# Optimization experiments

Measured on AMD Instinct MI355X. Metric: run time of the kernel, lower is better.

Reference implementation:

```python
import jax, jax.numpy as jnp
import numpy as np

K = 32            # neighbors per node
LAMBDA_REG = 0.1  # geodesic regularization weight
TEMP = 0.1        # softmax temperature


def setup_inputs() -> dict:
    key = jax.random.key(0)
    features = jax.random.normal(key, (8192, 128), dtype=jnp.float32)
    return {"features": features}


def reference(features):
    # features: [B, D]
    B, D = features.shape
    k = K

    # cosine-normalized similarity (F.normalize with eps=1e-12)
    fnorm = jnp.linalg.norm(features, axis=1, keepdims=True)        # [B, 1]
    x = features / jnp.maximum(fnorm, 1e-12)
    sim = x @ x.T                                                    # [B, B]

    # dynamic kNN graph: top-(k+1), drop self (first column)
    _, topk_idx = jax.lax.top_k(sim, k + 1)                          # [B, k+1]
    dst = topk_idx[:, 1:].reshape(-1)                                # [B*k]
    src = jnp.repeat(jnp.arange(B), k)                               # [B*k]
    rows = jnp.concatenate([src, dst])                               # [2*B*k]
    cols = jnp.concatenate([dst, src])

    # symmetric degree normalization (deg computed from src only, as in torch)
    deg = jax.ops.segment_sum(jnp.ones(B * k, jnp.float32), src, num_segments=B)
    dis = jnp.where(deg > 0, 1.0 / jnp.sqrt(jnp.maximum(deg, 1.0)), 0.0)
    w = dis[rows] * dis[cols]                                        # [2*B*k]

    def spmm(v):
        # sparse COO matmul: duplicate (row,col) entries sum, matching torch sparse
        return jax.ops.segment_sum(v[cols] * w[:, None], rows, num_segments=B)

    diff1 = spmm(features)          # A @ features
    geodesic = spmm(diff1)          # A @ (A @ features)

    # pairwise cosine similarity features vs geodesic (torch eps=1e-8)
    gnorm = jnp.linalg.norm(geodesic, axis=1)                        # [B]
    denom = jnp.maximum(fnorm * gnorm[None, :], 1e-8)                # [B, B]
    cos = (features @ geodesic.T) / denom

    raw_weights = sim + LAMBDA_REG * cos
    weights = jax.nn.softmax(raw_weights / TEMP, axis=-1)            # [B, B]
    enhanced = weights @ features                                    # [B, D]
    return enhanced
```

## Files before the change

kernel.cpp:

```cpp
#include <hip/hip_runtime.h>
#include <hip/hip_bf16.h>

typedef unsigned short u16;
typedef unsigned int u32;
typedef __attribute__((ext_vector_type(8))) short bf16x8;
typedef __attribute__((ext_vector_type(4))) float f32x4;

#define LOG2E 1.4426950408889634f
#define B_N 8192
#define D_DIM 128
#define KNN 32
#define CAP_P 28
#define NPART 16
#define TAU 0.19f

__device__ __forceinline__ u16 f2b(float f) {
    unsigned u = __float_as_uint(f);
    unsigned r = (u + 0x7fffu + ((u >> 16) & 1u)) >> 16;
    return (u16)r;
}
__device__ __forceinline__ float b2f(u16 h) { return __uint_as_float((u32)h << 16); }

__device__ __forceinline__ f32x4 mfma16(bf16x8 a, bf16x8 b, f32x4 c) {
    return __builtin_amdgcn_mfma_f32_16x16x32_bf16(a, b, c, 0, 0, 0);
}

__device__ __forceinline__ size_t pk_off(int i, int d) {
    int T = i >> 5, r = ((i >> 4) & 1) * 4 + (d >> 5);
    int lane = ((d >> 3) & 3) * 16 + (i & 15);
    return ((size_t)((T * 8 + r) * 64 + lane)) * 8 + (d & 7);
}

__global__ __launch_bounds__(128) void prep_kernel(const float* __restrict__ f,
                                                   u16* __restrict__ xb, u16* __restrict__ xbp) {
    int i = blockIdx.x, d = threadIdx.x;
    float v = f[i * D_DIM + d];
    float ss = v * v;
#pragma unroll
    for (int m = 1; m < 64; m <<= 1) ss += __shfl_xor(ss, m, 64);
    __shared__ float wsum[2];
    if ((d & 63) == 0) wsum[d >> 6] = ss;
    __syncthreads();
    float nrm = sqrtf(wsum[0] + wsum[1]);
    u16 b = f2b(v / fmaxf(nrm, 1e-12f));
    xb[i * D_DIM + d] = b;
    xbp[pk_off(i, d)] = b;
}

__global__ __launch_bounds__(256) void vtp_kernel(const float* __restrict__ f, u16* __restrict__ vtp) {
    __shared__ u16 tile[32][130];
    int T = blockIdx.x, t = threadIdx.x;
    for (int idx = t; idx < 32 * 128; idx += 256) {
        int ir = idx >> 7, d = idx & 127;
        tile[ir][d] = f2b(f[(size_t)(T * 32 + ir) * D_DIM + d]);
    }
    __syncthreads();
#pragma unroll
    for (int cc = 0; cc < 2; cc++) {
        int c = t + cc * 256;
        int db = c >> 6, lane = c & 63;
        u16 out[8];
#pragma unroll
        for (int j = 0; j < 8; j++)
            out[j] = tile[(lane >> 4) * 8 + j][db * 16 + (lane & 15)];
        *(bf16x8*)(vtp + (size_t)(T * 512 + c) * 8) = *(bf16x8*)out;
    }
}

__global__ __launch_bounds__(512, 1) void cand_kernel(const u16* __restrict__ xb, const u16* __restrict__ xbp,
                                                      u32* __restrict__ candk, int* __restrict__ candcnt) {
    __shared__ int cnt_s[256];
    int tid = threadIdx.x;
    int wave = tid >> 6, lane = tid & 63, l15 = lane & 15, l4 = lane >> 4;
    int part = blockIdx.y;
    int qrow0 = blockIdx.x * 256 + wave * 32;
    if (tid < 256) cnt_s[tid] = 0;
    __syncthreads();

    bf16x8 a[2][4];
#pragma unroll
    for (int rt = 0; rt < 2; rt++) {
        const u16* arow = xb + (size_t)(qrow0 + rt * 16 + l15) * D_DIM + l4 * 8;
#pragma unroll
        for (int kk = 0; kk < 4; kk++) a[rt][kk] = *(const bf16x8*)(arow + kk * 32);
    }

    auto ldb = [&](bf16x8 (&bfr)[2][4], int j0) {
        const u16* bp = xbp + ((size_t)(j0 >> 5) * 8) * 512 + lane * 8;
#pragma unroll
        for (int ct = 0; ct < 2; ct++)
#pragma unroll
            for (int kk = 0; kk < 4; kk++) bfr[ct][kk] = *(const bf16x8*)(bp + (ct * 4 + kk) * 512);
    };
    auto proc = [&](bf16x8 (&bfr)[2][4], int j0) {
#pragma unroll
        for (int rt = 0; rt < 2; rt++) {
            f32x4 s0 = {0.f, 0.f, 0.f, 0.f}, s1 = {0.f, 0.f, 0.f, 0.f};
#pragma unroll
            for (int kk = 0; kk < 4; kk++) {
                s0 = mfma16(a[rt][kk], bfr[0][kk], s0);
                s1 = mfma16(a[rt][kk], bfr[1][kk], s1);
            }
#pragma unroll
            for (int r = 0; r < 4; r++) {
                int rloc = wave * 32 + rt * 16 + 4 * l4 + r;
                int gi = blockIdx.x * 256 + rloc;
#pragma unroll
                for (int ct = 0; ct < 2; ct++) {
                    float v = ct ? s1[r] : s0[r];
                    int gj = j0 + ct * 16 + l15;
                    if (v >= TAU && gj != gi) {
                        int slot = atomicAdd(&cnt_s[rloc], 1);
                        if (slot < CAP_P) {
                            u32 key = ((u32)f2b(v) << 13) | (u32)(8191 - gj);
                            candk[((size_t)gi * NPART + part) * CAP_P + slot] = key;
                        }
                    }
                }
            }
        }
    };

    int jbeg = part * 512;
    bf16x8 bfrA[2][4], bfrB[2][4];
    ldb(bfrA, jbeg);
    for (int i = 0; i < 16; i += 2) {
        ldb(bfrB, jbeg + 32 * (i + 1));
        proc(bfrA, jbeg + 32 * i);
        if (i + 2 < 16) ldb(bfrA, jbeg + 32 * (i + 2));
        proc(bfrB, jbeg + 32 * (i + 1));
    }
    __syncthreads();
    if (tid < 256) candcnt[(blockIdx.x * 256 + tid) * NPART + part] = min(cnt_s[tid], CAP_P);
}

__global__ __launch_bounds__(512) void select_kernel(const u32* __restrict__ candk,
                                                     const int* __restrict__ candcnt,
                                                     int* __restrict__ nbr) {
    int wave = threadIdx.x >> 6, lane = threadIdx.x & 63;
    int row = blockIdx.x * 8 + wave;
    u32 k[7];
#pragma unroll
    for (int s = 0; s < 7; s++) {
        int idx = lane + 64 * s;
        int pp = idx / CAP_P, off = idx - pp * CAP_P;
        int cnt = candcnt[row * NPART + pp];
        u32 kk = candk[((size_t)row * NPART + pp) * CAP_P + off];
        k[s] = (off < cnt) ? kk : 0u;
    }
    for (int t = 0; t < KNN; t++) {
        u32 bk = k[0];
#pragma unroll
        for (int s = 1; s < 7; s++) bk = max(bk, k[s]);
#pragma unroll
        for (int m = 1; m < 64; m <<= 1) {
            u32 ok = (u32)__shfl_xor((int)bk, m, 64);
            bk = max(bk, ok);
        }
        int bi = 8191 - (int)(bk & 8191u);
        if (bk == 0u) bi = row;
        if (lane == 0) nbr[(size_t)row * KNN + t] = bi;
#pragma unroll
        for (int s = 0; s < 7; s++)
            if (k[s] == bk) k[s] = 0u;
    }
}

__global__ __launch_bounds__(256) void deg_kernel(const int* __restrict__ nbr, int* __restrict__ indeg) {
    int e = blockIdx.x * 256 + threadIdx.x;
    atomicAdd(&indeg[nbr[e]], 1);
}

__global__ __launch_bounds__(256) void scan_kernel(const int* __restrict__ indeg,
                                                   int* __restrict__ offsets, int* __restrict__ cursor) {
    __shared__ int ps[256];
    int t = threadIdx.x;
    int loc[32];
    int s = 0;
#pragma unroll
    for (int kq = 0; kq < 32; kq++) { loc[kq] = indeg[t * 32 + kq]; s += loc[kq]; }
    ps[t] = s;
    __syncthreads();
    for (int d = 1; d < 256; d <<= 1) {
        int vv = (t >= d) ? ps[t - d] : 0;
        __syncthreads();
        ps[t] += vv;
        __syncthreads();
    }
    int run = (t > 0) ? ps[t - 1] : 0;
#pragma unroll
    for (int kq = 0; kq < 32; kq++) {
        offsets[t * 32 + kq] = run;
        cursor[t * 32 + kq] = run;
        run += loc[kq];
    }
    if (t == 255) offsets[B_N] = run;
}

__global__ __launch_bounds__(256) void fill_kernel(const int* __restrict__ nbr,
                                                   int* __restrict__ cursor, int* __restrict__ rev) {
    int e = blockIdx.x * 256 + threadIdx.x;
    int j = nbr[e];
    int pos = atomicAdd(&cursor[j], 1);
    rev[pos] = e >> 5;
}

__global__ __launch_bounds__(128) void spmm_kernel(const float* __restrict__ in, float* __restrict__ outv,
                                                   const int* __restrict__ nbr, const int* __restrict__ offsets,
                                                   const int* __restrict__ rev) {
    int i = blockIdx.x, d = threadIdx.x;
    float acc = 0.f;
#pragma unroll 4
    for (int kq = 0; kq < KNN; kq++) acc += in[(size_t)nbr[i * KNN + kq] * D_DIM + d];
    int b0 = offsets[i], e0 = offsets[i + 1];
    for (int pp = b0; pp < e0; pp++) acc += in[(size_t)rev[pp] * D_DIM + d];
    outv[(size_t)i * D_DIM + d] = acc * (1.0f / 32.0f);
}

__global__ __launch_bounds__(128) void yb_kernel(const float* __restrict__ f, const float* __restrict__ geod,
                                                 u16* __restrict__ ybp) {
    int i = blockIdx.x, d = threadIdx.x;
    float fv = f[(size_t)i * D_DIM + d];
    float g = geod[(size_t)i * D_DIM + d];
    float sf = fv * fv, sg = g * g;
#pragma unroll
    for (int m = 1; m < 64; m <<= 1) {
        sf += __shfl_xor(sf, m, 64);
        sg += __shfl_xor(sg, m, 64);
    }
    __shared__ float wf[2], wg[2];
    if ((d & 63) == 0) { wf[d >> 6] = sf; wg[d >> 6] = sg; }
    __syncthreads();
    float fn = sqrtf(wf[0] + wf[1]);
    float gn = sqrtf(wg[0] + wg[1]);
    float yv = fv / fmaxf(fn, 1e-12f) + 0.1f * g / fmaxf(gn, 1e-12f);
    ybp[pk_off(i, d)] = f2b(yv);
}

__global__ __launch_bounds__(512, 1) void attn_kernel(const u16* __restrict__ xb, const u16* __restrict__ ybp,
                                                      const u16* __restrict__ vtp,
                                                      u16* __restrict__ Og, float* __restrict__ lg) {
    __shared__ u16 p_lds[8][32][40];
    int tid = threadIdx.x, wave = tid >> 6, lane = tid & 63, l15 = lane & 15, l4 = lane >> 4;
    int part = blockIdx.y;
    int qrow0 = blockIdx.x * 256 + wave * 32;

    bf16x8 qa[2][4];
#pragma unroll
    for (int rt = 0; rt < 2; rt++) {
        const u16* qrow = xb + (size_t)(qrow0 + rt * 16 + l15) * D_DIM + l4 * 8;
#pragma unroll
        for (int kk = 0; kk < 4; kk++) qa[rt][kk] = *(const bf16x8*)(qrow + kk * 32);
    }

    f32x4 O[2][8];
    float lrun[2][4];
#pragma unroll
    for (int rt = 0; rt < 2; rt++) {
#pragma unroll
        for (int db = 0; db < 8; db++) O[rt][db] = (f32x4){0.f, 0.f, 0.f, 0.f};
#pragma unroll
        for (int r = 0; r < 4; r++) lrun[rt][r] = 0.f;
    }

    const float SC = 10.0f * LOG2E;
    const float SH = 11.0f * LOG2E;
    int swz = l4 << 3;
    int rswz = ((l15 >> 2) & 3) << 3;

    auto ldy = [&](bf16x8 (&yf)[2][4], int kv0) {
        const u16* yp = ybp + ((size_t)(kv0 >> 5) * 8) * 512 + lane * 8;
#pragma unroll
        for (int ct = 0; ct < 2; ct++)
#pragma unroll
            for (int kk = 0; kk < 4; kk++) yf[ct][kk] = *(const bf16x8*)(yp + (ct * 4 + kk) * 512);
    };
    auto tile = [&](bf16x8 (&yf)[2][4], int kv0) {
        const u16* vp = vtp + ((size_t)(kv0 >> 5) * 8) * 512 + lane * 8;
        bf16x8 vf[8];
#pragma unroll
        for (int db = 0; db < 8; db++) vf[db] = *(const bf16x8*)(vp + db * 512);
#pragma unroll
        for (int rt = 0; rt < 2; rt++) {
            f32x4 s0 = {0.f, 0.f, 0.f, 0.f}, s1 = {0.f, 0.f, 0.f, 0.f};
#pragma unroll
            for (int kk = 0; kk < 4; kk++) {
                s0 = mfma16(qa[rt][kk], yf[0][kk], s0);
                s1 = mfma16(qa[rt][kk], yf[1][kk], s1);
            }
#pragma unroll
            for (int r = 0; r < 4; r++) {
                float p0 = exp2f(s0[r] * SC - SH);
                float p1 = exp2f(s1[r] * SC - SH);
                lrun[rt][r] += p0 + p1;
                int row = rt * 16 + 4 * l4 + r;
                p_lds[wave][row][l15 ^ swz] = f2b(p0);
                p_lds[wave][row][(16 + l15) ^ swz] = f2b(p1);
            }
        }
        bf16x8 pa[2];
#pragma unroll
        for (int rt = 0; rt < 2; rt++)
            pa[rt] = *(const bf16x8*)&p_lds[wave][rt * 16 + l15][(l4 * 8) ^ rswz];
#pragma unroll
        for (int db = 0; db < 8; db++) {
#pragma unroll
            for (int rt = 0; rt < 2; rt++) O[rt][db] = mfma16(pa[rt], vf[db], O[rt][db]);
        }
    };

    int kvbeg = part * 1024;
    bf16x8 yfA[2][4], yfB[2][4];
    ldy(yfA, kvbeg);
    for (int i = 0; i < 32; i += 2) {
        ldy(yfB, kvbeg + 32 * (i + 1));
        tile(yfA, kvbeg + 32 * i);
        if (i + 2 < 32) ldy(yfA, kvbeg + 32 * (i + 2));
        tile(yfB, kvbeg + 32 * (i + 1));
    }

#pragma unroll
    for (int rt = 0; rt < 2; rt++)
#pragma unroll
        for (int r = 0; r < 4; r++) {
            float s = lrun[rt][r];
#pragma unroll
            for (int m = 1; m < 16; m <<= 1) s += __shfl_xor(s, m, 64);
            if (l15 == 0) lg[part * B_N + qrow0 + rt * 16 + 4 * l4 + r] = s;
        }
#pragma unroll
    for (int rt = 0; rt < 2; rt++)
#pragma unroll
        for (int db = 0; db < 8; db++)
#pragma unroll
            for (int r = 0; r < 4; r++)
                Og[(size_t)part * B_N * D_DIM +
                   (size_t)(qrow0 + rt * 16 + 4 * l4 + r) * D_DIM + db * 16 + l15] = f2b(O[rt][db][r]);
}

__global__ __launch_bounds__(256) void norm_kernel(const u16* __restrict__ Og, const float* __restrict__ lg,
                                                   float* __restrict__ outp) {
    int idx = blockIdx.x * 256 + threadIdx.x;
    int row = idx >> 4;
    float acc[8] = {0.f, 0.f, 0.f, 0.f, 0.f, 0.f, 0.f, 0.f};
    float L = 0.f;
#pragma unroll
    for (int p = 0; p < 8; p++) {
        L += lg[p * B_N + row];
        bf16x8 v = *(const bf16x8*)(Og + (size_t)p * B_N * D_DIM + (size_t)idx * 8);
#pragma unroll
        for (int j = 0; j < 8; j++) acc[j] += b2f((u16)v[j]);
    }
    float inv = 1.0f / L;
#pragma unroll
    for (int j = 0; j < 8; j++) outp[(size_t)idx * 8 + j] = acc[j] * inv;
}

extern "C" void kernel_launch(void* const* d_in, const int* in_sizes, int n_in,
                              void* d_out, int out_size, void* d_ws, size_t ws_size,
                              hipStream_t stream) {
    const float* f = (const float*)d_in[0];
    float* outp = (float*)d_out;

    const size_t MB = 1u << 20;
    char* p = (char*)d_ws;
    auto alloc = [&](size_t n) -> char* {
        char* r = p;
        p += (n + 255) & ~(size_t)255;
        return r;
    };
    char* S = alloc(19 * MB);
    u16* xb = (u16*)alloc((size_t)B_N * D_DIM * 2);
    u16* ybp = (u16*)alloc((size_t)B_N * D_DIM * 2);
    u16* vtp = (u16*)alloc((size_t)B_N * D_DIM * 2);
    int* nbr = (int*)alloc((size_t)B_N * KNN * 4);
    int* rev = (int*)alloc((size_t)B_N * KNN * 4);
    int* indeg = (int*)alloc((size_t)B_N * 4);
    int* offsets = (int*)alloc((size_t)(B_N + 1) * 4);
    int* cursor = (int*)alloc((size_t)B_N * 4);
    int* candcnt = (int*)alloc((size_t)B_N * NPART * 4);
    float* lg = (float*)alloc((size_t)8 * B_N * 4);

    u32* candk = (u32*)S;
    float* diff1 = (float*)S;
    float* geod = (float*)(S + 4 * MB);
    u16* xbp = (u16*)(S + 15 * MB);
    u16* Og = (u16*)S;

    prep_kernel<<<B_N, 128, 0, stream>>>(f, xb, xbp);
    vtp_kernel<<<256, 256, 0, stream>>>(f, vtp);
    cand_kernel<<<dim3(32, NPART), 512, 0, stream>>>(xb, xbp, candk, candcnt);
    select_kernel<<<B_N / 8, 512, 0, stream>>>(candk, candcnt, nbr);
    hipMemsetAsync(indeg, 0, (size_t)B_N * 4, stream);
    deg_kernel<<<(B_N * KNN) / 256, 256, 0, stream>>>(nbr, indeg);
    scan_kernel<<<1, 256, 0, stream>>>(indeg, offsets, cursor);
    fill_kernel<<<(B_N * KNN) / 256, 256, 0, stream>>>(nbr, cursor, rev);
    spmm_kernel<<<B_N, 128, 0, stream>>>(f, diff1, nbr, offsets, rev);
    spmm_kernel<<<B_N, 128, 0, stream>>>(diff1, geod, nbr, offsets, rev);
    yb_kernel<<<B_N, 128, 0, stream>>>(f, geod, ybp);
    attn_kernel<<<dim3(32, 8), 512, 0, stream>>>(xb, ybp, vtp, Og, lg);
    norm_kernel<<<(B_N * D_DIM / 8) / 256, 256, 0, stream>>>(Og, lg, outp);
}
```

Baseline: 254.0 us.

## Stage key/value tiles through double-buffered LDS in cand and attn kernels

Both the candidate-scoring and attention kernels used to have every wave load the same packed B/Y/V tile fragments straight from global memory into registers. Now all 512 threads cooperatively fetch each 32-column tile once per block into a double-buffered shared-memory stage, prefetching the next tile into registers while the current one is computed. Waves then read their fragments from LDS, cutting redundant global/L2 traffic eightfold. The cost is a block-wide barrier every tile and extra LDS reads and writes, which can reduce the overlap between waves.

```diff
diff --git a/kernel.cpp b/kernel.cpp
--- a/kernel.cpp
+++ b/kernel.cpp
@@ -69,13 +69,13 @@
 
 __global__ __launch_bounds__(512, 1) void cand_kernel(const u16* __restrict__ xb, const u16* __restrict__ xbp,
                                                       u32* __restrict__ candk, int* __restrict__ candcnt) {
+    __shared__ u16 stage[2][4096];
     __shared__ int cnt_s[256];
     int tid = threadIdx.x;
     int wave = tid >> 6, lane = tid & 63, l15 = lane & 15, l4 = lane >> 4;
     int part = blockIdx.y;
     int qrow0 = blockIdx.x * 256 + wave * 32;
     if (tid < 256) cnt_s[tid] = 0;
-    __syncthreads();
 
     bf16x8 a[2][4];
 #pragma unroll
@@ -85,14 +85,26 @@
         for (int kk = 0; kk < 4; kk++) a[rt][kk] = *(const bf16x8*)(arow + kk * 32);
     }
 
-    auto ldb = [&](bf16x8 (&bfr)[2][4], int j0) {
-        const u16* bp = xbp + ((size_t)(j0 >> 5) * 8) * 512 + lane * 8;
+    int T0 = part * 16;
+    {
+        bf16x8 dx = *(const bf16x8*)(xbp + (size_t)T0 * 4096 + tid * 8);
+        *(bf16x8*)&stage[0][tid * 8] = dx;
+    }
+    __syncthreads();
+
+    int buf = 0;
+    for (int t = 0; t < 16; t++) {
+        bf16x8 dx;
+        bool pf = (t + 1 < 16);
+        if (pf) dx = *(const bf16x8*)(xbp + (size_t)(T0 + t + 1) * 4096 + tid * 8);
+
+        int j0 = part * 512 + t * 32;
+        bf16x8 bfr[2][4];
 #pragma unroll
         for (int ct = 0; ct < 2; ct++)
 #pragma unroll
-            for (int kk = 0; kk < 4; kk++) bfr[ct][kk] = *(const bf16x8*)(bp + (ct * 4 + kk) * 512);
-    };
-    auto proc = [&](bf16x8 (&bfr)[2][4], int j0) {
+            for (int kk = 0; kk < 4; kk++)
+                bfr[ct][kk] = *(const bf16x8*)&stage[buf][(ct * 4 + kk) * 512 + lane * 8];
 #pragma unroll
         for (int rt = 0; rt < 2; rt++) {
             f32x4 s0 = {0.f, 0.f, 0.f, 0.f}, s1 = {0.f, 0.f, 0.f, 0.f};
@@ -119,18 +131,10 @@
                 }
             }
         }
-    };
-
-    int jbeg = part * 512;
-    bf16x8 bfrA[2][4], bfrB[2][4];
-    ldb(bfrA, jbeg);
-    for (int i = 0; i < 16; i += 2) {
-        ldb(bfrB, jbeg + 32 * (i + 1));
-        proc(bfrA, jbeg + 32 * i);
-        if (i + 2 < 16) ldb(bfrA, jbeg + 32 * (i + 2));
-        proc(bfrB, jbeg + 32 * (i + 1));
-    }
-    __syncthreads();
+        if (pf) *(bf16x8*)&stage[buf ^ 1][tid * 8] = dx;
+        __syncthreads();
+        buf ^= 1;
+    }
     if (tid < 256) candcnt[(blockIdx.x * 256 + tid) * NPART + part] = min(cnt_s[tid], CAP_P);
 }
 
@@ -240,6 +244,7 @@
 __global__ __launch_bounds__(512, 1) void attn_kernel(const u16* __restrict__ xb, const u16* __restrict__ ybp,
                                                       const u16* __restrict__ vtp,
                                                       u16* __restrict__ Og, float* __restrict__ lg) {
+    __shared__ u16 stage[2][8192];
     __shared__ u16 p_lds[8][32][40];
     int tid = threadIdx.x, wave = tid >> 6, lane = tid & 63, l15 = lane & 15, l4 = lane >> 4;
     int part = blockIdx.y;
@@ -268,18 +273,36 @@
     int swz = l4 << 3;
     int rswz = ((l15 >> 2) & 3) << 3;
 
-    auto ldy = [&](bf16x8 (&yf)[2][4], int kv0) {
-        const u16* yp = ybp + ((size_t)(kv0 >> 5) * 8) * 512 + lane * 8;
+    int T0 = part * 32;
+    {
+        size_t g = (size_t)T0 * 4096 + tid * 8;
+        bf16x8 dy = *(const bf16x8*)(ybp + g);
+        bf16x8 dv = *(const bf16x8*)(vtp + g);
+        *(bf16x8*)&stage[0][tid * 8] = dy;
+        *(bf16x8*)&stage[0][4096 + tid * 8] = dv;
+    }
+    __syncthreads();
+
+    int buf = 0;
+    for (int t = 0; t < 32; t++) {
+        bf16x8 dy, dv;
+        bool pf = (t + 1 < 32);
+        if (pf) {
+            size_t g = (size_t)(T0 + t + 1) * 4096 + tid * 8;
+            dy = *(const bf16x8*)(ybp + g);
+            dv = *(const bf16x8*)(vtp + g);
+        }
+
+        bf16x8 vf[8];
+#pragma unroll
+        for (int db = 0; db < 8; db++)
+            vf[db] = *(const bf16x8*)&stage[buf][4096 + db * 512 + lane * 8];
+        bf16x8 yf[2][4];
 #pragma unroll
         for (int ct = 0; ct < 2; ct++)
 #pragma unroll
-            for (int kk = 0; kk < 4; kk++) yf[ct][kk] = *(const bf16x8*)(yp + (ct * 4 + kk) * 512);
-    };
-    auto tile = [&](bf16x8 (&yf)[2][4], int kv0) {
-        const u16* vp = vtp + ((size_t)(kv0 >> 5) * 8) * 512 + lane * 8;
-        bf16x8 vf[8];
-#pragma unroll
-        for (int db = 0; db < 8; db++) vf[db] = *(const bf16x8*)(vp + db * 512);
+            for (int kk = 0; kk < 4; kk++)
+                yf[ct][kk] = *(const bf16x8*)&stage[buf][(ct * 4 + kk) * 512 + lane * 8];
 #pragma unroll
         for (int rt = 0; rt < 2; rt++) {
             f32x4 s0 = {0.f, 0.f, 0.f, 0.f}, s1 = {0.f, 0.f, 0.f, 0.f};
@@ -307,16 +330,13 @@
 #pragma unroll
             for (int rt = 0; rt < 2; rt++) O[rt][db] = mfma16(pa[rt], vf[db], O[rt][db]);
         }
-    };
-
-    int kvbeg = part * 1024;
-    bf16x8 yfA[2][4], yfB[2][4];
-    ldy(yfA, kvbeg);
-    for (int i = 0; i < 32; i += 2) {
-        ldy(yfB, kvbeg + 32 * (i + 1));
-        tile(yfA, kvbeg + 32 * i);
-        if (i + 2 < 32) ldy(yfA, kvbeg + 32 * (i + 2));
-        tile(yfB, kvbeg + 32 * (i + 1));
+
+        if (pf) {
+            *(bf16x8*)&stage[buf ^ 1][tid * 8] = dy;
+            *(bf16x8*)&stage[buf ^ 1][4096 + tid * 8] = dv;
+        }
+        __syncthreads();
+        buf ^= 1;
     }
 
 #pragma unroll
```

Measured after the change: 233.4 us. -8.1%, faster.
